# Kernel tuning notes

Measured on AMD Instinct MI355X. Metric: run time of the kernel, lower is better.

## Reference

```python
import jax, jax.numpy as jnp
import numpy as np

DIM = 1024
HEADS = 16
HEAD_DIM = DIM // HEADS
FF = 4 * DIM


def setup_inputs() -> dict:
    key = jax.random.key(0)
    ks = jax.random.split(key, 16)
    s = 0.02
    return {
        "x": jax.random.normal(ks[0], (2, 2048, DIM), dtype=jnp.float32),
        "wq": jax.random.normal(ks[1], (DIM, DIM), dtype=jnp.float32) * s,
        "bq": jnp.zeros((DIM,), jnp.float32),
        "wk": jax.random.normal(ks[2], (DIM, DIM), dtype=jnp.float32) * s,
        "bk": jnp.zeros((DIM,), jnp.float32),
        "wv": jax.random.normal(ks[3], (DIM, DIM), dtype=jnp.float32) * s,
        "bv": jnp.zeros((DIM,), jnp.float32),
        "wo": jax.random.normal(ks[4], (DIM, DIM), dtype=jnp.float32) * s,
        "bo": jnp.zeros((DIM,), jnp.float32),
        "w1": jax.random.normal(ks[5], (DIM, FF), dtype=jnp.float32) * s,
        "b1": jnp.zeros((FF,), jnp.float32),
        "w2": jax.random.normal(ks[6], (FF, DIM), dtype=jnp.float32) * s,
        "b2": jnp.zeros((DIM,), jnp.float32),
        "g1": jnp.ones((DIM,), jnp.float32),
        "be1": jnp.zeros((DIM,), jnp.float32),
        "g2": jnp.ones((DIM,), jnp.float32),
        "be2": jnp.zeros((DIM,), jnp.float32),
    }


def _layernorm(x, g, b, eps=1e-5):
    mu = jnp.mean(x, axis=-1, keepdims=True)
    var = jnp.mean(jnp.square(x - mu), axis=-1, keepdims=True)
    return (x - mu) * jax.lax.rsqrt(var + eps) * g + b


def reference(x, wq, bq, wk, bk, wv, bv, wo, bo, w1, b1, w2, b2, g1, be1, g2, be2):
    B, T, D = x.shape
    normed = _layernorm(x, g1, be1)
    # [B,T,D] -> [B,H,T,hd]
    def heads(y):
        return y.reshape(B, T, HEADS, HEAD_DIM).transpose(0, 2, 1, 3)
    q = heads(normed @ wq + bq)
    k = heads(normed @ wk + bk)
    v = heads(normed @ wv + bv)
    scale = 1.0 / np.sqrt(HEAD_DIM).astype(np.float32)
    attn = jax.nn.softmax(jnp.einsum('bhqd,bhkd->bhqk', q, k) * scale, axis=-1)
    out = jnp.einsum('bhqk,bhkd->bhqd', attn, v)
    out = out.transpose(0, 2, 1, 3).reshape(B, T, D)
    x = x + out @ wo + bo
    h = _layernorm(x, g2, be2)
    ffn = jax.nn.gelu(h @ w1 + b1, approximate=False) @ w2 + b2
    return x + ffn
```

## Files before the change

kernel.cpp:

```cpp
#include <hip/hip_runtime.h>
#include <math.h>

#define DIM   1024
#define HEADS 16
#define HDIM  64
#define FFDIM 4096
#define MROWS 4096
#define SEQ   2048
#define QKVS  3072
#define SCALE_Q 0.1803368801111204f

typedef _Float16 f16x8 __attribute__((ext_vector_type(8)));
typedef _Float16 f16x4 __attribute__((ext_vector_type(4)));
typedef float    f32x4 __attribute__((ext_vector_type(4)));

#define GLOAD_LDS16(g, l) __builtin_amdgcn_global_load_lds(                 \
    (const __attribute__((address_space(1))) void*)(g),                     \
    (__attribute__((address_space(3))) void*)(l), 16, 0, 0)

__device__ __forceinline__ float gelu_exact(float x) {
    return 0.5f * x * (1.0f + erff(x * 0.70710678118654752f));
}

__device__ __forceinline__ int pk2(float a, float b) {
    union { _Float16 h[2]; int i; } u;
    u.h[0] = (_Float16)a; u.h[1] = (_Float16)b;
    return u.i;
}

__global__ __launch_bounds__(256) void ln_kernel(
    const float* __restrict__ x, const float* __restrict__ g,
    const float* __restrict__ b, _Float16* __restrict__ out)
{
    const int row = blockIdx.x;
    const int t   = threadIdx.x;
    const float4* xr = reinterpret_cast<const float4*>(x + (size_t)row * DIM);
    float4 v = xr[t];
    float s  = v.x + v.y + v.z + v.w;
    float ss = v.x*v.x + v.y*v.y + v.z*v.z + v.w*v.w;
    #pragma unroll
    for (int off = 32; off; off >>= 1) {
        s  += __shfl_down(s,  off);
        ss += __shfl_down(ss, off);
    }
    __shared__ float red[8];
    const int wave = t >> 6, lane = t & 63;
    if (lane == 0) { red[wave] = s; red[4 + wave] = ss; }
    __syncthreads();
    if (t == 0) {
        float S  = red[0] + red[1] + red[2] + red[3];
        float SS = red[4] + red[5] + red[6] + red[7];
        float mu  = S * (1.0f / DIM);
        float var = SS * (1.0f / DIM) - mu * mu;
        red[0] = mu;
        red[1] = rsqrtf(var + 1e-5f);
    }
    __syncthreads();
    const float mu = red[0], inv = red[1];
    const float4 gv = reinterpret_cast<const float4*>(g)[t];
    const float4 bv = reinterpret_cast<const float4*>(b)[t];
    f16x4 o;
    o[0] = (_Float16)((v.x - mu) * inv * gv.x + bv.x);
    o[1] = (_Float16)((v.y - mu) * inv * gv.y + bv.y);
    o[2] = (_Float16)((v.z - mu) * inv * gv.z + bv.z);
    o[3] = (_Float16)((v.w - mu) * inv * gv.w + bv.w);
    *reinterpret_cast<f16x4*>(out + (size_t)row * DIM + t * 4) = o;
}

__global__ void concat3(const float* __restrict__ a, const float* __restrict__ b,
                        const float* __restrict__ c, float* __restrict__ dst)
{
    const int i = blockIdx.x * 256 + threadIdx.x;
    if (i < 1024)      dst[i] = a[i];
    else if (i < 2048) dst[i] = b[i - 1024];
    else               dst[i] = c[i - 2048];
}

__global__ __launch_bounds__(256) void transpose_cvt(
    const float* __restrict__ src, _Float16* __restrict__ dst,
    int R, int C, int dstOff)
{
    __shared__ float t[32][33];
    const int c0 = blockIdx.x * 32, r0 = blockIdx.y * 32;
    const int tx = threadIdx.x & 31, ty = (threadIdx.x >> 5) * 4;
    #pragma unroll
    for (int i = 0; i < 4; ++i)
        t[ty + i][tx] = src[(size_t)(r0 + ty + i) * C + c0 + tx];
    __syncthreads();
    #pragma unroll
    for (int i = 0; i < 4; ++i)
        dst[(size_t)(dstOff + c0 + ty + i) * R + r0 + tx] = (_Float16)t[tx][ty + i];
}

__global__ __launch_bounds__(256) void transpose_cvt3(
    const float* __restrict__ s0, const float* __restrict__ s1,
    const float* __restrict__ s2, _Float16* __restrict__ dst)
{
    __shared__ float t[32][33];
    const float* src = blockIdx.z == 0 ? s0 : (blockIdx.z == 1 ? s1 : s2);
    const int dstOff = blockIdx.z * 1024;
    const int c0 = blockIdx.x * 32, r0 = blockIdx.y * 32;
    const int tx = threadIdx.x & 31, ty = (threadIdx.x >> 5) * 4;
    #pragma unroll
    for (int i = 0; i < 4; ++i)
        t[ty + i][tx] = src[(size_t)(r0 + ty + i) * 1024 + c0 + tx];
    __syncthreads();
    #pragma unroll
    for (int i = 0; i < 4; ++i)
        dst[(size_t)(dstOff + c0 + ty + i) * 1024 + r0 + tx] = (_Float16)t[tx][ty + i];
}

template<int EPI, int BM>
__global__ __launch_bounds__(256) void gemm_mfma(
    const _Float16* __restrict__ A,
    const _Float16* __restrict__ Bt,
    const float* __restrict__ bias,
    const float* __restrict__ res,
    float* __restrict__ Cf,
    _Float16* __restrict__ Ch,
    _Float16* __restrict__ Qh, _Float16* __restrict__ Kh,
    _Float16* __restrict__ Vtp,
    int M, int N, int K)
{
    constexpr int MF  = BM / 32;
    constexpr int ACH = BM / 64;
    __shared__ __attribute__((aligned(16))) _Float16 SMEM[8192];
    _Float16* As = SMEM;
    _Float16* Bs = SMEM + BM * 32;

    const int tid  = threadIdx.x;
    const int wave = tid >> 6;
    const int lane = tid & 63;
    const int bm = blockIdx.y * BM;
    const int bn = blockIdx.x * 128;
    const int wr = wave >> 1, wc = wave & 1;

    const int srow = lane >> 2;
    const int skc  = lane & 3;
    const _Float16* Ag = A  + (size_t)(bm + wave * ACH * 16 + srow) * K + skc * 8;
    const _Float16* Bg = Bt + (size_t)(bn + wave * 32 + srow) * K + skc * 8;
    _Float16* Al = As + wave * ACH * 512;
    _Float16* Bl = Bs + wave * 1024;

    f32x4 acc[MF][4] = {};

    const int fr = lane & 15;
    const int fk = (lane >> 4) * 8;

    for (int k0 = 0; k0 < K; k0 += 32) {
        __syncthreads();
        #pragma unroll
        for (int c = 0; c < ACH; ++c)
            GLOAD_LDS16(Ag + k0 + (size_t)c * 16 * K, Al + c * 512);
        GLOAD_LDS16(Bg + k0,                  Bl);
        GLOAD_LDS16(Bg + k0 + 16 * (size_t)K, Bl + 512);
        __syncthreads();

        f16x8 af[MF], bfr[4];
        #pragma unroll
        for (int m = 0; m < MF; ++m)
            af[m] = *reinterpret_cast<const f16x8*>(As + (wr * (BM/2) + m * 16 + fr) * 32 + fk);
        #pragma unroll
        for (int n = 0; n < 4; ++n)
            bfr[n] = *reinterpret_cast<const f16x8*>(Bs + (wc * 64 + n * 16 + fr) * 32 + fk);
        #pragma unroll
        for (int m = 0; m < MF; ++m)
            #pragma unroll
            for (int n = 0; n < 4; ++n)
                acc[m][n] = __builtin_amdgcn_mfma_f32_16x16x32_f16(
                    af[m], bfr[n], acc[m][n], 0, 0, 0);
    }

    const int fg = lane >> 4;

    if constexpr (EPI == 1) {
        #pragma unroll
        for (int m = 0; m < MF; ++m) {
            const int row0 = bm + wr * (BM/2) + m * 16 + fg * 4;
            #pragma unroll
            for (int n = 0; n < 4; ++n) {
                const int col = bn + wc * 64 + n * 16 + fr;
                const float bv = bias[col];
                #pragma unroll
                for (int j = 0; j < 4; ++j) {
                    const size_t idx = (size_t)(row0 + j) * N + col;
                    Cf[idx] = acc[m][n][j] + bv + res[idx];
                }
            }
        }
        return;
    }

    _Float16* wtile = SMEM + wave * 2048;

    const int sect = bn >> 10;
    const int bidx = bm >> 11;
    const int t0w  = (bm & 2047) + wr * (BM / 2);
    const int hh   = ((bn & 1023) >> 6) + wc;
    const size_t bh = (size_t)(bidx * 16 + hh);

    #pragma unroll
    for (int pass = 0; pass < MF / 2; ++pass) {
        __syncthreads();
        #pragma unroll
        for (int mi = 0; mi < 2; ++mi) {
            const int mm = pass * 2 + mi;
            #pragma unroll
            for (int n = 0; n < 4; ++n) {
                const int cl = n * 16 + fr;
                const float bv = bias[bn + wc * 64 + cl];
                #pragma unroll
                for (int j = 0; j < 4; ++j) {
                    const int rl = mi * 16 + fg * 4 + j;
                    float v = acc[mm][n][j] + bv;
                    _Float16 hv;
                    if constexpr (EPI == 2) hv = (_Float16)gelu_exact(v);
                    else hv = (_Float16)(sect == 0 ? v * SCALE_Q : v);
                    wtile[rl * 64 + ((((cl >> 3) ^ (rl & 7))) << 3) + (cl & 7)] = hv;
                }
            }
        }
        __syncthreads();

        if constexpr (EPI == 2) {
            _Float16* dst = Ch + (size_t)(bm + wr * (BM/2) + pass * 32) * N
                               + bn + wc * 64;
            #pragma unroll
            for (int it = 0; it < 4; ++it) {
                const int rl = it * 8 + (lane >> 3);
                const int ch = lane & 7;
                f16x8 vv = *reinterpret_cast<const f16x8*>(
                    wtile + rl * 64 + ((ch ^ (rl & 7)) << 3));
                *reinterpret_cast<f16x8*>(dst + (size_t)rl * N + ch * 8) = vv;
            }
        } else {
            if (sect < 2) {
                _Float16* dst = (sect == 0 ? Qh : Kh)
                              + (bh * 2048 + t0w + pass * 32) * 64;
                #pragma unroll
                for (int it = 0; it < 4; ++it) {
                    const int rl = it * 8 + (lane >> 3);
                    const int ch = lane & 7;
                    f16x8 vv = *reinterpret_cast<const f16x8*>(
                        wtile + rl * 64 + ((ch ^ (rl & 7)) << 3));
                    *reinterpret_cast<f16x8*>(dst + (size_t)rl * 64 + ch * 8) = vv;
                }
            } else {
                _Float16* dst = Vtp + bh * (64 * 2048) + t0w + pass * 32;
                #pragma unroll
                for (int it = 0; it < 4; ++it) {
                    const int d   = it * 16 + (lane >> 2);
                    const int tch = lane & 3;
                    f16x8 vv;
                    #pragma unroll
                    for (int u = 0; u < 8; ++u) {
                        const int rl = tch * 8 + u;
                        vv[u] = wtile[rl * 64 + (((d >> 3) ^ (rl & 7)) << 3) + (d & 7)];
                    }
                    *reinterpret_cast<f16x8*>(dst + (size_t)d * 2048 + tch * 8) = vv;
                }
            }
        }
    }
}

__global__ __launch_bounds__(256) void attn_mfma(
    const _Float16* __restrict__ Qh, const _Float16* __restrict__ Kh,
    const _Float16* __restrict__ Vt, _Float16* __restrict__ O)
{
    __shared__ __attribute__((aligned(16))) _Float16 Kbuf[2][4096];
    __shared__ __attribute__((aligned(16))) _Float16 Vbuf[2][4096];

    const int fid = blockIdx.x;
    const int qt  = (fid >> 3) & 31;
    const int bh  = (fid & 7) * 4 + (fid >> 8);

    const int tid  = threadIdx.x;
    const int w    = tid >> 6;
    const int lane = tid & 63;
    const int fr   = lane & 15;
    const int g    = lane >> 4;

    const int srow_lo = lane >> 3;
    const int sc      = (lane & 7) ^ (srow_lo & 7);
    const int rowA = w * 8 + srow_lo;
    const int rowB = (w + 4) * 8 + srow_lo;
    const char* Kg = (const char*)(Kh + (size_t)bh * (2048 * 64));
    const char* Vg = (const char*)(Vt + (size_t)bh * (64 * 2048));

#define STAGE(nb, kt) do {                                                   \
    GLOAD_LDS16(Kg + ((size_t)(((kt) * 64 + rowA)) << 7) + (sc << 4),        \
                &Kbuf[nb][w * 512]);                                         \
    GLOAD_LDS16(Kg + ((size_t)(((kt) * 64 + rowB)) << 7) + (sc << 4),        \
                &Kbuf[nb][(w + 4) * 512]);                                   \
    GLOAD_LDS16(Vg + ((size_t)rowA << 12) + ((kt) << 7) + (sc << 4),         \
                &Vbuf[nb][w * 512]);                                         \
    GLOAD_LDS16(Vg + ((size_t)rowB << 12) + ((kt) << 7) + (sc << 4),         \
                &Vbuf[nb][(w + 4) * 512]);                                   \
} while (0)

    const int qrow = qt * 64 + w * 16 + fr;
    const f16x8* Qp = reinterpret_cast<const f16x8*>(
        Qh + ((size_t)bh * 2048 + qrow) * 64);
    const f16x8 qf0 = Qp[g];
    const f16x8 qf1 = Qp[4 + g];

    const int fr7 = fr & 7;
    const int cs0 = ((g ^ fr7) << 4);
    const int cs1 = (((4 + g) ^ fr7) << 4);

    f32x4 o[4] = {};
    float mrun = -INFINITY, l = 0.0f;

    const int idx0 = (fr + ((g & 1) << 5)) << 2;
    const int idx1 = idx0 + 64;
    const bool ghi = (g >= 2);

    STAGE(0, 0);
    __syncthreads();
    int cur = 0;

    for (int kt = 0; kt < 32; ++kt) {
        if (kt < 31) STAGE(cur ^ 1, kt + 1);

        f32x4 sT[4] = {};
        {
            const char* Kb = (const char*)Kbuf[cur];
            #pragma unroll
            for (int mm = 0; mm < 4; ++mm) {
                const char* rb = Kb + ((mm * 16 + fr) << 7);
                f16x8 ka = *reinterpret_cast<const f16x8*>(rb + cs0);
                f16x8 kb = *reinterpret_cast<const f16x8*>(rb + cs1);
                sT[mm] = __builtin_amdgcn_mfma_f32_16x16x32_f16(ka, qf0, sT[mm], 0, 0, 0);
                sT[mm] = __builtin_amdgcn_mfma_f32_16x16x32_f16(kb, qf1, sT[mm], 0, 0, 0);
            }
        }

        float pm = sT[0][0];
        #pragma unroll
        for (int mm = 0; mm < 4; ++mm)
            #pragma unroll
            for (int j = 0; j < 4; ++j) pm = fmaxf(pm, sT[mm][j]);
        pm = fmaxf(pm, __shfl_xor(pm, 16));
        pm = fmaxf(pm, __shfl_xor(pm, 32));
        if (!__all(pm - mrun <= 8.0f)) {
            const float mnew  = fmaxf(mrun, pm);
            const float alpha = exp2f(mrun - mnew);
            mrun = mnew;
            l *= alpha;
            #pragma unroll
            for (int mm = 0; mm < 4; ++mm)
                #pragma unroll
                for (int j = 0; j < 4; ++j) o[mm][j] *= alpha;
        }
        float rs = 0.0f;
        #pragma unroll
        for (int mm = 0; mm < 4; ++mm)
            #pragma unroll
            for (int j = 0; j < 4; ++j) {
                const float p = exp2f(sT[mm][j] - mrun);
                sT[mm][j] = p;
                rs += p;
            }
        rs += __shfl_xor(rs, 16);
        rs += __shfl_xor(rs, 32);
        l += rs;

        int pk[4][2];
        #pragma unroll
        for (int mm = 0; mm < 4; ++mm) {
            pk[mm][0] = pk2(sT[mm][0], sT[mm][1]);
            pk[mm][1] = pk2(sT[mm][2], sT[mm][3]);
        }

        union BF { int i[4]; f16x8 h; } bf0, bf1;
        #pragma unroll
        for (int s = 0; s < 2; ++s) {
            union BF* bf = s ? &bf1 : &bf0;
            const int rA = 2 * s, rB = 2 * s + 1;
            int a0 = __builtin_amdgcn_ds_bpermute(idx0, pk[rA][0]);
            int b0 = __builtin_amdgcn_ds_bpermute(idx0, pk[rB][0]);
            int a1 = __builtin_amdgcn_ds_bpermute(idx0, pk[rA][1]);
            int b1 = __builtin_amdgcn_ds_bpermute(idx0, pk[rB][1]);
            int a2 = __builtin_amdgcn_ds_bpermute(idx1, pk[rA][0]);
            int b2 = __builtin_amdgcn_ds_bpermute(idx1, pk[rB][0]);
            int a3 = __builtin_amdgcn_ds_bpermute(idx1, pk[rA][1]);
            int b3 = __builtin_amdgcn_ds_bpermute(idx1, pk[rB][1]);
            bf->i[0] = ghi ? b0 : a0;
            bf->i[1] = ghi ? b1 : a1;
            bf->i[2] = ghi ? b2 : a2;
            bf->i[3] = ghi ? b3 : a3;
        }

        {
            const char* Vb = (const char*)Vbuf[cur];
            #pragma unroll
            for (int mm = 0; mm < 4; ++mm) {
                const char* rb = Vb + ((mm * 16 + fr) << 7);
                f16x8 va = *reinterpret_cast<const f16x8*>(rb + cs0);
                f16x8 vb = *reinterpret_cast<const f16x8*>(rb + cs1);
                o[mm] = __builtin_amdgcn_mfma_f32_16x16x32_f16(va, bf0.h, o[mm], 0, 0, 0);
                o[mm] = __builtin_amdgcn_mfma_f32_16x16x32_f16(vb, bf1.h, o[mm], 0, 0, 0);
            }
        }

        __syncthreads();
        cur ^= 1;
    }
#undef STAGE

    const float linv = 1.0f / l;
    const int b = bh >> 4, h = bh & 15;
    _Float16* Op = O + (size_t)(b * 2048 + qt * 64 + w * 16 + fr) * DIM
                     + h * 64 + 4 * g;
    #pragma unroll
    for (int mm = 0; mm < 4; ++mm) {
        f16x4 st;
        #pragma unroll
        for (int j = 0; j < 4; ++j) st[j] = (_Float16)(o[mm][j] * linv);
        *reinterpret_cast<f16x4*>(Op + mm * 16) = st;
    }
}

extern "C" void kernel_launch(void* const* d_in, const int* in_sizes, int n_in,
                              void* d_out, int out_size, void* d_ws, size_t ws_size,
                              hipStream_t stream)
{
    const float* x   = (const float*)d_in[0];
    const float* wq  = (const float*)d_in[1];
    const float* bq  = (const float*)d_in[2];
    const float* wk  = (const float*)d_in[3];
    const float* bk  = (const float*)d_in[4];
    const float* wv  = (const float*)d_in[5];
    const float* bv  = (const float*)d_in[6];
    const float* wo  = (const float*)d_in[7];
    const float* bo  = (const float*)d_in[8];
    const float* w1  = (const float*)d_in[9];
    const float* b1  = (const float*)d_in[10];
    const float* w2  = (const float*)d_in[11];
    const float* b2  = (const float*)d_in[12];
    const float* g1  = (const float*)d_in[13];
    const float* be1 = (const float*)d_in[14];
    const float* g2  = (const float*)d_in[15];
    const float* be2 = (const float*)d_in[16];
    float* out = (float*)d_out;

    char* wsb = (char*)d_ws;
    _Float16* Wt     = (_Float16*)(wsb);
    _Float16* normed = (_Float16*)(wsb + ((size_t)8  << 20));
    _Float16* Qh     = (_Float16*)(wsb + ((size_t)16 << 20));
    _Float16* Kh     = (_Float16*)(wsb + ((size_t)24 << 20));
    _Float16* Vt     = (_Float16*)(wsb + ((size_t)32 << 20));
    _Float16* mid    = (_Float16*)(wsb + ((size_t)16 << 20));
    _Float16* attno  = (_Float16*)(wsb + ((size_t)40 << 20));
    float*    bqkv   = (float*)   (wsb + ((size_t)48 << 20));

    ln_kernel<<<MROWS, 256, 0, stream>>>(x, g1, be1, normed);
    concat3<<<12, 256, 0, stream>>>(bq, bk, bv, bqkv);
    transpose_cvt3<<<dim3(32, 32, 3), 256, 0, stream>>>(wq, wk, wv, Wt);
    gemm_mfma<3, 128><<<dim3(QKVS / 128, MROWS / 128), 256, 0, stream>>>(
        normed, Wt, bqkv, nullptr, nullptr, nullptr, Qh, Kh, Vt,
        MROWS, QKVS, DIM);
    attn_mfma<<<1024, 256, 0, stream>>>(Qh, Kh, Vt, attno);
    transpose_cvt<<<dim3(32, 32), 256, 0, stream>>>(wo, Wt, 1024, 1024, 0);
    gemm_mfma<1, 64><<<dim3(DIM / 128, MROWS / 64), 256, 0, stream>>>(
        attno, Wt, bo, x, out, nullptr, nullptr, nullptr, nullptr,
        MROWS, DIM, DIM);
    ln_kernel<<<MROWS, 256, 0, stream>>>(out, g2, be2, normed);
    transpose_cvt<<<dim3(128, 32), 256, 0, stream>>>(w1, Wt, 1024, 4096, 0);
    gemm_mfma<2, 128><<<dim3(FFDIM / 128, MROWS / 128), 256, 0, stream>>>(
        normed, Wt, b1, nullptr, nullptr, mid, nullptr, nullptr, nullptr,
        MROWS, FFDIM, DIM);
    transpose_cvt<<<dim3(32, 128), 256, 0, stream>>>(w2, Wt, 4096, 1024, 0);
    gemm_mfma<1, 64><<<dim3(DIM / 128, MROWS / 64), 256, 0, stream>>>(
        mid, Wt, b2, out, out, nullptr, nullptr, nullptr, nullptr,
        MROWS, DIM, FFDIM);
}
```

Baseline: 457.3 us.

## Fuse prep kernels, unify GEMM tile to 128 rows, use natural exp in softmax

New measurement: 454.1 us. No clear change (-0.7%).

```diff
diff --git a/kernel.cpp b/kernel.cpp
--- a/kernel.cpp
+++ b/kernel.cpp
@@ -8,7 +8,7 @@
 #define MROWS 4096
 #define SEQ   2048
 #define QKVS  3072
-#define SCALE_Q 0.1803368801111204f
+#define SCALE_Q 0.125f
 
 typedef _Float16 f16x8 __attribute__((ext_vector_type(8)));
 typedef _Float16 f16x4 __attribute__((ext_vector_type(4)));
@@ -28,12 +28,11 @@
     return u.i;
 }
 
-__global__ __launch_bounds__(256) void ln_kernel(
+__device__ __forceinline__ void ln_row(
     const float* __restrict__ x, const float* __restrict__ g,
-    const float* __restrict__ b, _Float16* __restrict__ out)
-{
-    const int row = blockIdx.x;
-    const int t   = threadIdx.x;
+    const float* __restrict__ b, _Float16* __restrict__ out,
+    int row, int t, float* red)
+{
     const float4* xr = reinterpret_cast<const float4*>(x + (size_t)row * DIM);
     float4 v = xr[t];
     float s  = v.x + v.y + v.z + v.w;
@@ -43,7 +42,6 @@
         s  += __shfl_down(s,  off);
         ss += __shfl_down(ss, off);
     }
-    __shared__ float red[8];
     const int wave = t >> 6, lane = t & 63;
     if (lane == 0) { red[wave] = s; red[4 + wave] = ss; }
     __syncthreads();
@@ -67,18 +65,57 @@
     *reinterpret_cast<f16x4*>(out + (size_t)row * DIM + t * 4) = o;
 }
 
-__global__ void concat3(const float* __restrict__ a, const float* __restrict__ b,
-                        const float* __restrict__ c, float* __restrict__ dst)
-{
-    const int i = blockIdx.x * 256 + threadIdx.x;
-    if (i < 1024)      dst[i] = a[i];
-    else if (i < 2048) dst[i] = b[i - 1024];
-    else               dst[i] = c[i - 2048];
+__global__ __launch_bounds__(256) void ln_kernel(
+    const float* __restrict__ x, const float* __restrict__ g,
+    const float* __restrict__ b, _Float16* __restrict__ out)
+{
+    __shared__ float red[8];
+    ln_row(x, g, b, out, blockIdx.x, threadIdx.x, red);
+}
+
+__global__ __launch_bounds__(256) void prep1(
+    const float* __restrict__ x, const float* __restrict__ g1,
+    const float* __restrict__ be1, _Float16* __restrict__ normed,
+    const float* __restrict__ bq, const float* __restrict__ bk,
+    const float* __restrict__ bv, float* __restrict__ bqkv,
+    const float* __restrict__ wq, const float* __restrict__ wk,
+    const float* __restrict__ wv, const float* __restrict__ wo,
+    _Float16* __restrict__ Wt)
+{
+    __shared__ float smem[32 * 33];
+    const int bid = blockIdx.x;
+    const int tid = threadIdx.x;
+    if (bid < 4096) {
+        ln_row(x, g1, be1, normed, bid, tid, smem);
+    } else if (bid < 4108) {
+        const int i = (bid - 4096) * 256 + tid;
+        if (i < 1024)      bqkv[i] = bq[i];
+        else if (i < 2048) bqkv[i] = bk[i - 1024];
+        else               bqkv[i] = bv[i - 2048];
+    } else {
+        const int tb    = bid - 4108;
+        const int which = tb >> 10;
+        const int t32   = tb & 1023;
+        const float* src = which == 0 ? wq : which == 1 ? wk
+                         : which == 2 ? wv : wo;
+        const int dstOff = which << 10;
+        const int c0 = (t32 & 31) * 32, r0 = (t32 >> 5) * 32;
+        const int tx = tid & 31, ty = (tid >> 5) * 4;
+        float (*t)[33] = reinterpret_cast<float (*)[33]>(smem);
+        #pragma unroll
+        for (int i = 0; i < 4; ++i)
+            t[ty + i][tx] = src[(size_t)(r0 + ty + i) * 1024 + c0 + tx];
+        __syncthreads();
+        #pragma unroll
+        for (int i = 0; i < 4; ++i)
+            Wt[(size_t)(dstOff + c0 + ty + i) * 1024 + r0 + tx] =
+                (_Float16)t[tx][ty + i];
+    }
 }
 
 __global__ __launch_bounds__(256) void transpose_cvt(
     const float* __restrict__ src, _Float16* __restrict__ dst,
-    int R, int C, int dstOff)
+    int R, int C)
 {
     __shared__ float t[32][33];
     const int c0 = blockIdx.x * 32, r0 = blockIdx.y * 32;
@@ -89,28 +126,10 @@
     __syncthreads();
     #pragma unroll
     for (int i = 0; i < 4; ++i)
-        dst[(size_t)(dstOff + c0 + ty + i) * R + r0 + tx] = (_Float16)t[tx][ty + i];
-}
-
-__global__ __launch_bounds__(256) void transpose_cvt3(
-    const float* __restrict__ s0, const float* __restrict__ s1,
-    const float* __restrict__ s2, _Float16* __restrict__ dst)
-{
-    __shared__ float t[32][33];
-    const float* src = blockIdx.z == 0 ? s0 : (blockIdx.z == 1 ? s1 : s2);
-    const int dstOff = blockIdx.z * 1024;
-    const int c0 = blockIdx.x * 32, r0 = blockIdx.y * 32;
-    const int tx = threadIdx.x & 31, ty = (threadIdx.x >> 5) * 4;
-    #pragma unroll
-    for (int i = 0; i < 4; ++i)
-        t[ty + i][tx] = src[(size_t)(r0 + ty + i) * 1024 + c0 + tx];
-    __syncthreads();
-    #pragma unroll
-    for (int i = 0; i < 4; ++i)
-        dst[(size_t)(dstOff + c0 + ty + i) * 1024 + r0 + tx] = (_Float16)t[tx][ty + i];
-}
-
-template<int EPI, int BM>
+        dst[(size_t)(c0 + ty + i) * R + r0 + tx] = (_Float16)t[tx][ty + i];
+}
+
+template<int EPI>
 __global__ __launch_bounds__(256) void gemm_mfma(
     const _Float16* __restrict__ A,
     const _Float16* __restrict__ Bt,
@@ -122,49 +141,47 @@
     _Float16* __restrict__ Vtp,
     int M, int N, int K)
 {
-    constexpr int MF  = BM / 32;
-    constexpr int ACH = BM / 64;
     __shared__ __attribute__((aligned(16))) _Float16 SMEM[8192];
     _Float16* As = SMEM;
-    _Float16* Bs = SMEM + BM * 32;
+    _Float16* Bs = SMEM + 4096;
 
     const int tid  = threadIdx.x;
     const int wave = tid >> 6;
     const int lane = tid & 63;
-    const int bm = blockIdx.y * BM;
+    const int bm = blockIdx.y * 128;
     const int bn = blockIdx.x * 128;
     const int wr = wave >> 1, wc = wave & 1;
 
+    const int c0   = wave * 2;
     const int srow = lane >> 2;
     const int skc  = lane & 3;
-    const _Float16* Ag = A  + (size_t)(bm + wave * ACH * 16 + srow) * K + skc * 8;
-    const _Float16* Bg = Bt + (size_t)(bn + wave * 32 + srow) * K + skc * 8;
-    _Float16* Al = As + wave * ACH * 512;
-    _Float16* Bl = Bs + wave * 1024;
-
-    f32x4 acc[MF][4] = {};
+    const _Float16* Ag = A  + (size_t)(bm + c0 * 16 + srow) * K + skc * 8;
+    const _Float16* Bg = Bt + (size_t)(bn + c0 * 16 + srow) * K + skc * 8;
+    _Float16* Al = As + c0 * 512;
+    _Float16* Bl = Bs + c0 * 512;
+
+    f32x4 acc[4][4] = {};
 
     const int fr = lane & 15;
     const int fk = (lane >> 4) * 8;
 
     for (int k0 = 0; k0 < K; k0 += 32) {
         __syncthreads();
-        #pragma unroll
-        for (int c = 0; c < ACH; ++c)
-            GLOAD_LDS16(Ag + k0 + (size_t)c * 16 * K, Al + c * 512);
+        GLOAD_LDS16(Ag + k0,                  Al);
+        GLOAD_LDS16(Ag + k0 + 16 * (size_t)K, Al + 512);
         GLOAD_LDS16(Bg + k0,                  Bl);
         GLOAD_LDS16(Bg + k0 + 16 * (size_t)K, Bl + 512);
         __syncthreads();
 
-        f16x8 af[MF], bfr[4];
-        #pragma unroll
-        for (int m = 0; m < MF; ++m)
-            af[m] = *reinterpret_cast<const f16x8*>(As + (wr * (BM/2) + m * 16 + fr) * 32 + fk);
+        f16x8 af[4], bfr[4];
+        #pragma unroll
+        for (int m = 0; m < 4; ++m)
+            af[m] = *reinterpret_cast<const f16x8*>(As + (wr * 64 + m * 16 + fr) * 32 + fk);
         #pragma unroll
         for (int n = 0; n < 4; ++n)
             bfr[n] = *reinterpret_cast<const f16x8*>(Bs + (wc * 64 + n * 16 + fr) * 32 + fk);
         #pragma unroll
-        for (int m = 0; m < MF; ++m)
+        for (int m = 0; m < 4; ++m)
             #pragma unroll
             for (int n = 0; n < 4; ++n)
                 acc[m][n] = __builtin_amdgcn_mfma_f32_16x16x32_f16(
@@ -175,8 +192,8 @@
 
     if constexpr (EPI == 1) {
         #pragma unroll
-        for (int m = 0; m < MF; ++m) {
-            const int row0 = bm + wr * (BM/2) + m * 16 + fg * 4;
+        for (int m = 0; m < 4; ++m) {
+            const int row0 = bm + wr * 64 + m * 16 + fg * 4;
             #pragma unroll
             for (int n = 0; n < 4; ++n) {
                 const int col = bn + wc * 64 + n * 16 + fr;
@@ -195,12 +212,12 @@
 
     const int sect = bn >> 10;
     const int bidx = bm >> 11;
-    const int t0w  = (bm & 2047) + wr * (BM / 2);
+    const int t0w  = (bm & 2047) + wr * 64;
     const int hh   = ((bn & 1023) >> 6) + wc;
     const size_t bh = (size_t)(bidx * 16 + hh);
 
     #pragma unroll
-    for (int pass = 0; pass < MF / 2; ++pass) {
+    for (int pass = 0; pass < 2; ++pass) {
         __syncthreads();
         #pragma unroll
         for (int mi = 0; mi < 2; ++mi) {
@@ -223,7 +240,7 @@
         __syncthreads();
 
         if constexpr (EPI == 2) {
-            _Float16* dst = Ch + (size_t)(bm + wr * (BM/2) + pass * 32) * N
+            _Float16* dst = Ch + (size_t)(bm + wr * 64 + pass * 32) * N
                                + bn + wc * 64;
             #pragma unroll
             for (int it = 0; it < 4; ++it) {
@@ -345,7 +362,7 @@
         pm = fmaxf(pm, __shfl_xor(pm, 32));
         if (!__all(pm - mrun <= 8.0f)) {
             const float mnew  = fmaxf(mrun, pm);
-            const float alpha = exp2f(mrun - mnew);
+            const float alpha = __expf(mrun - mnew);
             mrun = mnew;
             l *= alpha;
             #pragma unroll
@@ -358,7 +375,7 @@
         for (int mm = 0; mm < 4; ++mm)
             #pragma unroll
             for (int j = 0; j < 4; ++j) {
-                const float p = exp2f(sT[mm][j] - mrun);
+                const float p = __expf(sT[mm][j] - mrun);
                 sT[mm][j] = p;
                 rs += p;
             }
@@ -455,24 +472,22 @@
     _Float16* attno  = (_Float16*)(wsb + ((size_t)40 << 20));
     float*    bqkv   = (float*)   (wsb + ((size_t)48 << 20));
 
-    ln_kernel<<<MROWS, 256, 0, stream>>>(x, g1, be1, normed);
-    concat3<<<12, 256, 0, stream>>>(bq, bk, bv, bqkv);
-    transpose_cvt3<<<dim3(32, 32, 3), 256, 0, stream>>>(wq, wk, wv, Wt);
-    gemm_mfma<3, 128><<<dim3(QKVS / 128, MROWS / 128), 256, 0, stream>>>(
+    prep1<<<8204, 256, 0, stream>>>(x, g1, be1, normed, bq, bk, bv, bqkv,
+                                    wq, wk, wv, wo, Wt);
+    gemm_mfma<3><<<dim3(QKVS / 128, MROWS / 128), 256, 0, stream>>>(
         normed, Wt, bqkv, nullptr, nullptr, nullptr, Qh, Kh, Vt,
         MROWS, QKVS, DIM);
     attn_mfma<<<1024, 256, 0, stream>>>(Qh, Kh, Vt, attno);
-    transpose_cvt<<<dim3(32, 32), 256, 0, stream>>>(wo, Wt, 1024, 1024, 0);
-    gemm_mfma<1, 64><<<dim3(DIM / 128, MROWS / 64), 256, 0, stream>>>(
-        attno, Wt, bo, x, out, nullptr, nullptr, nullptr, nullptr,
-        MROWS, DIM, DIM);
+    gemm_mfma<1><<<dim3(DIM / 128, MROWS / 128), 256, 0, stream>>>(
+        attno, Wt + (size_t)3072 * 1024, bo, x, out, nullptr,
+        nullptr, nullptr, nullptr, MROWS, DIM, DIM);
     ln_kernel<<<MROWS, 256, 0, stream>>>(out, g2, be2, normed);
-    transpose_cvt<<<dim3(128, 32), 256, 0, stream>>>(w1, Wt, 1024, 4096, 0);
-    gemm_mfma<2, 128><<<dim3(FFDIM / 128, MROWS / 128), 256, 0, stream>>>(
+    transpose_cvt<<<dim3(128, 32), 256, 0, stream>>>(w1, Wt, 1024, 4096);
+    gemm_mfma<2><<<dim3(FFDIM / 128, MROWS / 128), 256, 0, stream>>>(
         normed, Wt, b1, nullptr, nullptr, mid, nullptr, nullptr, nullptr,
         MROWS, FFDIM, DIM);
-    transpose_cvt<<<dim3(32, 128), 256, 0, stream>>>(w2, Wt, 4096, 1024, 0);
-    gemm_mfma<1, 64><<<dim3(DIM / 128, MROWS / 64), 256, 0, stream>>>(
+    transpose_cvt<<<dim3(32, 128), 256, 0, stream>>>(w2, Wt, 4096, 1024);
+    gemm_mfma<1><<<dim3(DIM / 128, MROWS / 128), 256, 0, stream>>>(
         mid, Wt, b2, out, out, nullptr, nullptr, nullptr, nullptr,
         MROWS, DIM, FFDIM);
 }
```
